# Kernel tuning notes

Measured on AMD Instinct MI355X. Metric: run time of the kernel, lower is better.

Reference implementation:

```python
import jax, jax.numpy as jnp
import numpy as np

T = 2048          # tokens (single-sequence prefill)
HID = 4096        # hidden_size
NH = 32           # num attention heads
NKV = 8           # num kv heads (GQA)
HD = 128          # head_dim
QKV_OUT = (NH + 2 * NKV) * HD  # 6144
THETA = 10000.0
SCALING = HD ** -0.5


def setup_inputs() -> dict:
    key = jax.random.key(0)
    ks = jax.random.split(key, 8)
    positions = jnp.arange(T, dtype=jnp.int32)
    # per-token int8 quantized hidden states (symmetric, [-127,127])
    q_act = jax.random.randint(ks[0], (T, HID), -127, 128, dtype=jnp.int32)
    # per-token dynamic activation scale
    act_scale = jax.random.uniform(ks[1], (T,), jnp.float32) * 0.01 + 0.001
    # int4 weights stored unsigned [0,15] with per-output-channel scale & zero point
    w_qkv_q = jax.random.randint(ks[2], (QKV_OUT, HID), 0, 16, dtype=jnp.int32)
    w_qkv_scale = jax.random.uniform(ks[3], (QKV_OUT,), jnp.float32) * 0.01 + 0.001
    w_qkv_zero = jax.random.uniform(ks[4], (QKV_OUT,), jnp.float32) * 2.0 + 7.0
    w_o_q = jax.random.randint(ks[5], (HID, HID), 0, 16, dtype=jnp.int32)
    w_o_scale = jax.random.uniform(ks[6], (HID,), jnp.float32) * 0.01 + 0.001
    w_o_zero = jax.random.uniform(ks[7], (HID,), jnp.float32) * 2.0 + 7.0
    return dict(positions=positions, q_act=q_act, act_scale=act_scale,
                w_qkv_q=w_qkv_q, w_qkv_scale=w_qkv_scale, w_qkv_zero=w_qkv_zero,
                w_o_q=w_o_q, w_o_scale=w_o_scale, w_o_zero=w_o_zero)


def w4a8_linear(qa_f, s_a, a_sum, qw, s_w, z_w):
    # y[t,o] = s_a[t]*s_w[o] * ( (qa @ qw^T)[t,o] - z_w[o]*sum_j qa[t,j] )
    acc = jnp.matmul(qa_f, qw.astype(jnp.float32).T)  # [T, O]
    return (s_a[:, None] * s_w[None, :]) * (acc - z_w[None, :] * a_sum[:, None])


def apply_rope(x, positions):
    # neox-style RoPE over full head_dim
    half = HD // 2
    inv_freq = THETA ** (-jnp.arange(0, half, dtype=jnp.float32) / half * 1.0)
    inv_freq = 1.0 / (THETA ** (jnp.arange(0, HD, 2, dtype=jnp.float32) / HD))
    freqs = positions.astype(jnp.float32)[:, None] * inv_freq[None, :]  # [T, HD/2]
    cos = jnp.cos(freqs)[:, None, :]
    sin = jnp.sin(freqs)[:, None, :]
    x1, x2 = x[..., :half], x[..., half:]
    return jnp.concatenate([x1 * cos - x2 * sin, x2 * cos + x1 * sin], axis=-1)


def dynamic_quant_with_sum(x):
    # per-token symmetric int8 dynamic quantization + fused sum
    s = jnp.maximum(jnp.max(jnp.abs(x), axis=-1), 1e-8) / 127.0  # [T]
    q = jnp.clip(jnp.round(x / s[:, None]), -127, 127)
    return q, s, jnp.sum(q, axis=-1)


def reference(positions, q_act, act_scale, w_qkv_q, w_qkv_scale, w_qkv_zero,
              w_o_q, w_o_scale, w_o_zero):
    qa_f = q_act.astype(jnp.float32)
    a_sum = jnp.sum(qa_f, axis=-1)  # fused activation sum
    qkv = w4a8_linear(qa_f, act_scale, a_sum, w_qkv_q, w_qkv_scale, w_qkv_zero)
    q, k, v = jnp.split(qkv, [NH * HD, NH * HD + NKV * HD], axis=-1)
    q = q.reshape(T, NH, HD)
    k = k.reshape(T, NKV, HD)
    v = v.reshape(T, NKV, HD)
    q = apply_rope(q, positions)
    k = apply_rope(k, positions)
    # GQA: repeat kv heads
    rep = NH // NKV
    k = jnp.repeat(k, rep, axis=1)  # [T, NH, HD]
    v = jnp.repeat(v, rep, axis=1)
    scores = jnp.einsum('qhd,khd->hqk', q, k) * SCALING  # [NH, T, T]
    causal = jnp.tril(jnp.ones((T, T), dtype=bool))
    scores = jnp.where(causal[None], scores, -jnp.inf)
    probs = jax.nn.softmax(scores, axis=-1)
    attn = jnp.einsum('hqk,khd->qhd', probs, v).reshape(T, NH * HD)
    # invoke_quant_fuse_sum: dynamic per-token quantization of attn output
    q2, s2, sum2 = dynamic_quant_with_sum(attn)
    out = w4a8_linear(q2, s2, sum2, w_o_q, w_o_scale, w_o_zero)
    return out
```

## Files before the change

kernel.cpp:

```cpp
#include <hip/hip_runtime.h>

#define T 2048
#define HID 4096
#define NH 32
#define NKV 8
#define HD 128
#define QKV_OUT ((NH + 2*NKV) * HD)
#define SCALING 0.08838834764831843f
#define QS2 0.12751744954f
#define DEFER_THR 10.0f
#define ROPE_C 0.20762050593046014f

typedef __attribute__((ext_vector_type(8))) short bfrag;
typedef __attribute__((ext_vector_type(4))) float ffrag;
typedef __attribute__((ext_vector_type(4))) int  ifrag;
typedef __attribute__((ext_vector_type(16))) char c16;

__device__ __forceinline__ short f2bf(float f) {
  unsigned u = __builtin_bit_cast(unsigned, f);
  u += 0x7fffu + ((u >> 16) & 1u);
  return (short)(u >> 16);
}

__device__ __forceinline__ void split2(float x, short& hi, short& lo) {
  unsigned u = __builtin_bit_cast(unsigned, x);
  unsigned uh = u + (0x7fffu + ((u >> 16) & 1u));
  hi = (short)(uh >> 16);
  float fh = __builtin_bit_cast(float, uh & 0xffff0000u);
  float r = x - fh;
  unsigned ur = __builtin_bit_cast(unsigned, r);
  ur += 0x7fffu + ((ur >> 16) & 1u);
  lo = (short)(ur >> 16);
}

__device__ __forceinline__ void gload_lds16(const void* g, void* l) {
  __builtin_amdgcn_global_load_lds(
      (const __attribute__((address_space(1))) unsigned int*)g,
      (__attribute__((address_space(3))) unsigned int*)l, 16, 0, 0);
}

__global__ __launch_bounds__(256)
void asum_conv(const int* __restrict__ qact, float* __restrict__ a_sum,
               char* __restrict__ a_i8) {
  __shared__ int red[256];
  const int t = blockIdx.x, tid = threadIdx.x;
  const int* row = qact + (size_t)t * HID + tid * 16;
  int s = 0;
  c16 o;
#pragma unroll
  for (int i = 0; i < 4; i++) {
    int4 v = *(const int4*)(row + i * 4);
    s += v.x + v.y + v.z + v.w;
    o[i*4+0] = (char)v.x; o[i*4+1] = (char)v.y;
    o[i*4+2] = (char)v.z; o[i*4+3] = (char)v.w;
  }
  *(c16*)(a_i8 + (size_t)t * HID + tid * 16) = o;
  red[tid] = s; __syncthreads();
  for (int off = 128; off > 0; off >>= 1) {
    if (tid < off) red[tid] += red[tid + off];
    __syncthreads();
  }
  if (tid == 0) a_sum[t] = (float)red[0];
}

__global__ __launch_bounds__(256)
void conv_i2c(const int* __restrict__ src, char* __restrict__ dst, int n16) {
  int idx = blockIdx.x * 256 + threadIdx.x;
  if (idx >= n16) return;
  const int4* s4 = (const int4*)src + (size_t)idx * 4;
  c16 o;
#pragma unroll
  for (int j = 0; j < 4; j++) {
    int4 v = s4[j];
    o[j*4+0] = (char)v.x; o[j*4+1] = (char)v.y;
    o[j*4+2] = (char)v.z; o[j*4+3] = (char)v.w;
  }
  *(c16*)(dst + (size_t)idx * 16) = o;
}

__global__ __launch_bounds__(256)
void gemm_i8(const char* __restrict__ A, const char* __restrict__ W,
             const float* __restrict__ s_a, const float* __restrict__ asum,
             const float* __restrict__ s_w, const float* __restrict__ z_w,
             float* __restrict__ C, int M, int N, int K) {
  __shared__ __align__(16) char As[128 * 64];
  __shared__ __align__(16) char Bs[128 * 64];
  const int tid = threadIdx.x;
  const int lane = tid & 63;
  const int quad = lane >> 4, l15 = lane & 15;
  const int wave = tid >> 6;
  const int wm = (wave >> 1) * 64, wn = (wave & 1) * 64;
  const int bm = blockIdx.y * 128, bn = blockIdx.x * 128;
  const int sr = tid >> 2, sc = (tid & 3) * 16;

  ifrag acc[4][4];
#pragma unroll
  for (int mi = 0; mi < 4; mi++)
#pragma unroll
    for (int ni = 0; ni < 4; ni++)
      acc[mi][ni] = (ifrag){0, 0, 0, 0};

  for (int k0 = 0; k0 < K; k0 += 64) {
#pragma unroll
    for (int it = 0; it < 2; it++) {
      gload_lds16(A + (size_t)(bm + it * 64 + sr) * K + k0 + sc,
                  &As[it * 4096 + wave * 1024]);
      gload_lds16(W + (size_t)(bn + it * 64 + sr) * K + k0 + sc,
                  &Bs[it * 4096 + wave * 1024]);
    }
    __syncthreads();

    ifrag af[4], bfv[4];
#pragma unroll
    for (int mi = 0; mi < 4; mi++)
      af[mi] = *(const ifrag*)&As[(wm + mi * 16 + l15) * 64 + quad * 16];
#pragma unroll
    for (int ni = 0; ni < 4; ni++)
      bfv[ni] = *(const ifrag*)&Bs[(wn + ni * 16 + l15) * 64 + quad * 16];
#pragma unroll
    for (int mi = 0; mi < 4; mi++)
#pragma unroll
      for (int ni = 0; ni < 4; ni++)
        acc[mi][ni] = __builtin_amdgcn_mfma_i32_16x16x64_i8(
            af[mi], bfv[ni], acc[mi][ni], 0, 0, 0);
    __syncthreads();
  }

#pragma unroll
  for (int mi = 0; mi < 4; mi++) {
    int row0 = bm + wm + mi * 16 + quad * 4;
#pragma unroll
    for (int r = 0; r < 4; r++) {
      int row = row0 + r;
      float sa = s_a[row], av = asum[row];
#pragma unroll
      for (int ni = 0; ni < 4; ni++) {
        int col = bn + wn + ni * 16 + l15;
        C[(size_t)row * N + col] = (sa * s_w[col]) * ((float)acc[mi][ni][r] - z_w[col] * av);
      }
    }
  }
}

__global__ __launch_bounds__(256)
void split_kv(float* __restrict__ qkv, const int* __restrict__ positions,
              short* __restrict__ Kh, short* __restrict__ Kl,
              short* __restrict__ Vth) {
  __shared__ __align__(16) short Vh_lds[128 * 72];
  const int y = blockIdx.y;
  const int t0 = blockIdx.x * 64;
  const int tid = threadIdx.x;

  if (y >= NKV) {
    const int h = y - NKV;
#pragma unroll
    for (int it = 0; it < 4; it++) {
      int c = tid + 256 * it;
      int key = c >> 4, dc = c & 15;
      float* qr = qkv + (size_t)(t0 + key) * QKV_OUT + (size_t)h * HD;
      float4 a = *(const float4*)(qr + dc * 4);
      float4 b = *(const float4*)(qr + dc * 4 + 64);
      float av[4] = {a.x, a.y, a.z, a.w};
      float bv[4] = {b.x, b.y, b.z, b.w};
      float pos = (float)positions[t0 + key];
#pragma unroll
      for (int jj = 0; jj < 4; jj++) {
        float fr = pos * exp2f(-ROPE_C * (float)(dc * 4 + jj));
        float sn, cs; sincosf(fr, &sn, &cs);
        float x1 = av[jj], x2 = bv[jj];
        av[jj] = x1 * cs - x2 * sn;
        bv[jj] = x2 * cs + x1 * sn;
      }
      *(float4*)(qr + dc * 4)      = make_float4(av[0], av[1], av[2], av[3]);
      *(float4*)(qr + dc * 4 + 64) = make_float4(bv[0], bv[1], bv[2], bv[3]);
    }
    return;
  }

  const int kvh = y;
#pragma unroll
  for (int it = 0; it < 4; it++) {
    int c = tid + 256 * it;
    int key = c >> 4, dc = c & 15;
    const int t = t0 + key;
    const float* kr = qkv + (size_t)t * QKV_OUT
                      + (size_t)NH * HD + (size_t)kvh * HD;
    float4 a = *(const float4*)(kr + dc * 4);
    float4 b = *(const float4*)(kr + dc * 4 + 64);
    float av[4] = {a.x, a.y, a.z, a.w};
    float bv[4] = {b.x, b.y, b.z, b.w};
    float pos = (float)positions[t];
    short4 ha, la, hb, lb;
    short hh, ll;
#pragma unroll
    for (int jj = 0; jj < 4; jj++) {
      float fr = pos * exp2f(-ROPE_C * (float)(dc * 4 + jj));
      float sn, cs; sincosf(fr, &sn, &cs);
      float x1 = av[jj], x2 = bv[jj];
      float r1 = x1 * cs - x2 * sn;
      float r2 = x2 * cs + x1 * sn;
      split2(r1, hh, ll); ((short*)&ha)[jj] = hh; ((short*)&la)[jj] = ll;
      split2(r2, hh, ll); ((short*)&hb)[jj] = hh; ((short*)&lb)[jj] = ll;
    }
    const int uu = ((dc >> 1) ^ t) & 7;
    const int h4 = (dc & 1) * 4;
    size_t base = (size_t)kvh * T * HD + (size_t)t * HD;
    *(short4*)(Kh + base + uu * 8 + h4) = ha;
    *(short4*)(Kl + base + uu * 8 + h4) = la;
    *(short4*)(Kh + base + (8 + uu) * 8 + h4) = hb;
    *(short4*)(Kl + base + (8 + uu) * 8 + h4) = lb;
  }
#pragma unroll
  for (int i = 0; i < 8; i++) {
    int c = tid + 256 * i;
    int key = c >> 5, dc = c & 31;
    float4 f = *(const float4*)(qkv + (size_t)(t0 + key) * QKV_OUT
                                + (size_t)(NH + NKV) * HD + (size_t)kvh * HD + dc * 4);
    Vh_lds[(dc*4+0)*72 + key] = f2bf(f.x);
    Vh_lds[(dc*4+1)*72 + key] = f2bf(f.y);
    Vh_lds[(dc*4+2)*72 + key] = f2bf(f.z);
    Vh_lds[(dc*4+3)*72 + key] = f2bf(f.w);
  }
  __syncthreads();
#pragma unroll
  for (int i = 0; i < 2; i++) {
    int c = tid + 256 * i;
    int row = c >> 2, cc = c & 3;
    int sd = (row >> 1) & 3;
    size_t o = (size_t)kvh * HD * T + (size_t)row * T + t0 + ((cc ^ sd)) * 8;
    *(bfrag*)(Vth + o) = *(const bfrag*)&Vh_lds[row * 72 + cc * 8];
  }
#pragma unroll
  for (int i = 0; i < 2; i++) {
    int c = tid + 256 * i;
    int row = c >> 2, cc = c & 3;
    int sd = (row >> 1) & 3;
    size_t o = (size_t)kvh * HD * T + (size_t)row * T + t0 + 32 + ((cc ^ sd)) * 8;
    *(bfrag*)(Vth + o) = *(const bfrag*)&Vh_lds[row * 72 + 32 + cc * 8];
  }
}

__global__ __launch_bounds__(256)
void attn_kernel(const float* __restrict__ qkv,
                 const short* __restrict__ Kh, const short* __restrict__ Kl,
                 const short* __restrict__ Vth,
                 float* __restrict__ attn) {
  __shared__ __align__(16) short Ksh[2][32 * 128];
  __shared__ __align__(16) short Ksl[2][32 * 128];
  __shared__ __align__(16) short Vsh[2][128 * 32];
  __shared__ __align__(16) short Psh[4 * 16 * 40];

  const int kvh = blockIdx.x & 7;
  const int pair = blockIdx.x >> 3;
  const int tid = threadIdx.x;
  const int lane = tid & 63;
  const int wv = tid >> 6;
  const int l15 = lane & 15, quad = lane >> 4;
  const int h = kvh * 4 + wv;
  short* Pw = Psh + wv * 16 * 40;

  const short* KhB = Kh + (size_t)kvh * T * HD;
  const short* KlB = Kl + (size_t)kvh * T * HD;
  const short* VhB = Vth + (size_t)kvh * HD * T;

  const int offK0 = (tid >> 4) * 128 + (tid & 15) * 8;
  const int offK1 = offK0 + 16 * 128;
  const int offV0 = (tid >> 2) * T + (tid & 3) * 8;
  const int offV1 = offV0 + 64 * T;
  const int wv1k = wv * 1024;

  auto stage = [&](int k0, int b) {
    const short* khs = KhB + (size_t)k0 * HD;
    const short* kls = KlB + (size_t)k0 * HD;
    const short* vs  = VhB + k0;
    gload_lds16(khs + offK0, (char*)&Ksh[b][0] + wv1k);
    gload_lds16(khs + offK1, (char*)&Ksh[b][0] + 4096 + wv1k);
    gload_lds16(kls + offK0, (char*)&Ksl[b][0] + wv1k);
    gload_lds16(kls + offK1, (char*)&Ksl[b][0] + 4096 + wv1k);
    gload_lds16(vs + offV0, (char*)&Vsh[b][0] + wv1k);
    gload_lds16(vs + offV1, (char*)&Vsh[b][0] + 4096 + wv1k);
  };

  const int sdv = (l15 >> 1) & 3;
  const int vq8 = (quad ^ sdv) * 8;
  int uuk[4];
#pragma unroll
  for (int kc = 0; kc < 4; kc++) {
    int s = 4 * kc + quad;
    uuk[kc] = ((s & 8) | ((s ^ l15) & 7)) * 8;
  }

  bfrag ones;
#pragma unroll
  for (int j = 0; j < 8; j++) ones[j] = (short)0x3f80;

  for (int pass = 0; pass < 2; pass++) {
    const int qt = pass ? pair : 127 - pair;
    const int q0 = qt * 16;
    const int nk = (q0 >> 5) + 1;

    bfrag qh[4], ql[4];
    const float* qrow = qkv + (size_t)(q0 + l15) * QKV_OUT + (size_t)h * HD;
#pragma unroll
    for (int kc = 0; kc < 4; kc++) {
      float4 f0 = *(const float4*)(qrow + kc * 32 + quad * 8);
      float4 f1 = *(const float4*)(qrow + kc * 32 + quad * 8 + 4);
      float fv[8] = {f0.x, f0.y, f0.z, f0.w, f1.x, f1.y, f1.z, f1.w};
#pragma unroll
      for (int j = 0; j < 8; j++) {
        short hi, lo; split2(fv[j] * QS2, hi, lo);
        qh[kc][j] = hi; ql[kc][j] = lo;
      }
    }

    ffrag o[8], ol;
    ol = (ffrag){0.f, 0.f, 0.f, 0.f};
#pragma unroll
    for (int n = 0; n < 8; n++) o[n] = (ffrag){0.f, 0.f, 0.f, 0.f};
    float m_i[4] = {-1e30f, -1e30f, -1e30f, -1e30f};

    stage(0, 0);
    asm volatile("s_waitcnt vmcnt(0)" ::: "memory");
    __builtin_amdgcn_s_barrier();

    int cur = 0;
    for (int kt = 0; kt < nk; kt++) {
      const int k0 = kt << 5;
      if (kt + 1 < nk) stage(k0 + 32, cur ^ 1);

      const short* ksh = &Ksh[cur][0];
      const short* ksl = &Ksl[cur][0];
      const short* vsh = &Vsh[cur][0];

      ffrag s[2];
      s[0] = (ffrag){0.f,0.f,0.f,0.f}; s[1] = (ffrag){0.f,0.f,0.f,0.f};
#pragma unroll
      for (int kc = 0; kc < 4; kc++) {
#pragma unroll
        for (int n = 0; n < 2; n++) {
          const int rb = (n * 16 + l15) * 128 + uuk[kc];
          bfrag bh = *(const bfrag*)&ksh[rb];
          bfrag bl = *(const bfrag*)&ksl[rb];
          s[n] = __builtin_amdgcn_mfma_f32_16x16x32_bf16(qh[kc], bh, s[n], 0,0,0);
          s[n] = __builtin_amdgcn_mfma_f32_16x16x32_bf16(qh[kc], bl, s[n], 0,0,0);
          s[n] = __builtin_amdgcn_mfma_f32_16x16x32_bf16(ql[kc], bh, s[n], 0,0,0);
        }
      }
      const bool lastkt = (kt == nk - 1);
      float sv[2][4];
#pragma unroll
      for (int n = 0; n < 2; n++)
#pragma unroll
        for (int r = 0; r < 4; r++) {
          float v = s[n][r];
          if (lastkt) {
            int key = k0 + n * 16 + l15;
            int row = q0 + quad * 4 + r;
            if (key > row) v = -1e30f;
          }
          sv[n][r] = v;
        }
      float lm[4];
      bool trig = false;
#pragma unroll
      for (int r = 0; r < 4; r++) {
        lm[r] = fmaxf(sv[0][r], sv[1][r]);
        trig = trig || (lm[r] > m_i[r] + DEFER_THR);
      }
      if (__any(trig)) {
#pragma unroll
        for (int r = 0; r < 4; r++) {
          float m2 = lm[r];
          m2 = fmaxf(m2, __shfl_xor(m2, 1));
          m2 = fmaxf(m2, __shfl_xor(m2, 2));
          m2 = fmaxf(m2, __shfl_xor(m2, 4));
          m2 = fmaxf(m2, __shfl_xor(m2, 8));
          float mn = fmaxf(m_i[r], m2);
          float a = exp2f(m_i[r] - mn);
          m_i[r] = mn;
          ol[r] *= a;
#pragma unroll
          for (int n = 0; n < 8; n++) o[n][r] *= a;
        }
      }
#pragma unroll
      for (int n = 0; n < 2; n++)
#pragma unroll
        for (int r = 0; r < 4; r++) {
          float p = exp2f(sv[n][r] - m_i[r]);
          Pw[(quad*4 + r) * 40 + n*16 + l15] = f2bf(p);
        }
      bfrag ph = *(const bfrag*)&Pw[l15 * 40 + quad * 8];
      ol = __builtin_amdgcn_mfma_f32_16x16x32_bf16(ph, ones, ol, 0,0,0);
#pragma unroll
      for (int n = 0; n < 8; n++) {
        bfrag vh = *(const bfrag*)&vsh[(n * 16 + l15) * 32 + vq8];
        o[n] = __builtin_amdgcn_mfma_f32_16x16x32_bf16(ph, vh, o[n], 0,0,0);
      }

      asm volatile("s_waitcnt vmcnt(0)" ::: "memory");
      __builtin_amdgcn_s_barrier();
      cur ^= 1;
    }

    float inv[4];
#pragma unroll
    for (int r = 0; r < 4; r++) inv[r] = 1.f / ol[r];
#pragma unroll
    for (int n = 0; n < 8; n++)
#pragma unroll
      for (int r = 0; r < 4; r++) {
        int row = q0 + quad * 4 + r;
        attn[(size_t)row * HID + (size_t)h * HD + n * 16 + l15] = o[n][r] * inv[r];
      }
  }
}

__global__ __launch_bounds__(256)
void quant_kernel(const float* __restrict__ x, char* __restrict__ q2,
                  float* __restrict__ s2, float* __restrict__ sum2) {
  __shared__ float red[256];
  const int t = blockIdx.x, tid = threadIdx.x;
  const float* row = x + (size_t)t * HID;
  float4 v[4];
  float m = 0.f;
#pragma unroll
  for (int i = 0; i < 4; i++) {
    v[i] = *(const float4*)(row + tid * 16 + i * 4);
    m = fmaxf(m, fmaxf(fmaxf(fabsf(v[i].x), fabsf(v[i].y)),
                       fmaxf(fabsf(v[i].z), fabsf(v[i].w))));
  }
  red[tid] = m; __syncthreads();
  for (int off = 128; off > 0; off >>= 1) {
    if (tid < off) red[tid] = fmaxf(red[tid], red[tid + off]);
    __syncthreads();
  }
  float s = fmaxf(red[0], 1e-8f) / 127.f;
  __syncthreads();
  float ssum = 0.f;
  c16 o;
#pragma unroll
  for (int i = 0; i < 4; i++) {
    float q;
    q = fminf(127.f, fmaxf(-127.f, rintf(v[i].x / s))); ssum += q; o[i*4+0] = (char)(int)q;
    q = fminf(127.f, fmaxf(-127.f, rintf(v[i].y / s))); ssum += q; o[i*4+1] = (char)(int)q;
    q = fminf(127.f, fmaxf(-127.f, rintf(v[i].z / s))); ssum += q; o[i*4+2] = (char)(int)q;
    q = fminf(127.f, fmaxf(-127.f, rintf(v[i].w / s))); ssum += q; o[i*4+3] = (char)(int)q;
  }
  *(c16*)(q2 + (size_t)t * HID + tid * 16) = o;
  red[tid] = ssum; __syncthreads();
  for (int off = 128; off > 0; off >>= 1) {
    if (tid < off) red[tid] += red[tid + off];
    __syncthreads();
  }
  if (tid == 0) { s2[t] = s; sum2[t] = red[0]; }
}

extern "C" void kernel_launch(void* const* d_in, const int* in_sizes, int n_in,
                              void* d_out, int out_size, void* d_ws, size_t ws_size,
                              hipStream_t stream) {
  const int*   positions   = (const int*)d_in[0];
  const int*   q_act       = (const int*)d_in[1];
  const float* act_scale   = (const float*)d_in[2];
  const int*   w_qkv_q     = (const int*)d_in[3];
  const float* w_qkv_scale = (const float*)d_in[4];
  const float* w_qkv_zero  = (const float*)d_in[5];
  const int*   w_o_q       = (const int*)d_in[6];
  const float* w_o_scale   = (const float*)d_in[7];
  const float* w_o_zero    = (const float*)d_in[8];
  float* out = (float*)d_out;

  size_t off = 0;
  auto alloc = [&](size_t bytes) -> void* {
    void* p = (char*)d_ws + off;
    off += (bytes + 255) & ~(size_t)255;
    return p;
  };
  float* qkv   = (float*)alloc((size_t)T * QKV_OUT * 4);
  char*  act8  = (char*)alloc((size_t)T * HID);
  char*  w8    = (char*)alloc((size_t)QKV_OUT * HID);
  short* Kh    = (short*)alloc((size_t)NKV * T * HD * 2);
  short* Kl    = (short*)alloc((size_t)NKV * T * HD * 2);
  short* Vth   = (short*)alloc((size_t)NKV * T * HD * 2);
  float* a_sum = (float*)alloc(T * 4);
  float* s2    = (float*)alloc(T * 4);
  float* sum2  = (float*)alloc(T * 4);
  (void)ws_size;

  asum_conv<<<T, 256, 0, stream>>>(q_act, a_sum, act8);
  conv_i2c<<<(QKV_OUT * HID / 16 + 255) / 256, 256, 0, stream>>>(
      w_qkv_q, w8, QKV_OUT * HID / 16);
  gemm_i8<<<dim3(QKV_OUT / 128, T / 128), 256, 0, stream>>>(
      act8, w8, act_scale, a_sum, w_qkv_scale, w_qkv_zero, qkv, T, QKV_OUT, HID);
  split_kv<<<dim3(T / 64, NKV + NH), 256, 0, stream>>>(qkv, positions, Kh, Kl, Vth);
  attn_kernel<<<dim3(512), 256, 0, stream>>>(qkv, Kh, Kl, Vth, out);
  conv_i2c<<<(HID * HID / 16 + 255) / 256, 256, 0, stream>>>(
      w_o_q, w8, HID * HID / 16);
  quant_kernel<<<T, 256, 0, stream>>>(out, act8, s2, sum2);
  gemm_i8<<<dim3(HID / 128, T / 128), 256, 0, stream>>>(
      act8, w8, s2, sum2, w_o_scale, w_o_zero, out, T, HID, HID);
}
```

Baseline: 522.3 us.

## Double GEMM K-tile to 128 with XOR-swizzled int8 layout; precompute RoPE table

```diff
diff --git a/kernel.cpp b/kernel.cpp
--- a/kernel.cpp
+++ b/kernel.cpp
@@ -40,6 +40,16 @@
 }
 
 __global__ __launch_bounds__(256)
+void rope_table(float2* __restrict__ tab) {
+  int idx = blockIdx.x * 256 + threadIdx.x;
+  int p = idx >> 6, j = idx & 63;
+  float fr = (float)p * exp2f(-ROPE_C * (float)j);
+  float sn, cs; sincosf(fr, &sn, &cs);
+  tab[idx] = make_float2(cs, sn);
+}
+
+
+__global__ __launch_bounds__(256)
 void asum_conv(const int* __restrict__ qact, float* __restrict__ a_sum,
                char* __restrict__ a_i8) {
   __shared__ int red[256];
@@ -54,7 +64,8 @@
     o[i*4+0] = (char)v.x; o[i*4+1] = (char)v.y;
     o[i*4+2] = (char)v.z; o[i*4+3] = (char)v.w;
   }
-  *(c16*)(a_i8 + (size_t)t * HID + tid * 16) = o;
+  const int chunk = (tid & ~7) | ((tid & 7) ^ (t & 7));
+  *(c16*)(a_i8 + (size_t)t * HID + chunk * 16) = o;
   red[tid] = s; __syncthreads();
   for (int off = 128; off > 0; off >>= 1) {
     if (tid < off) red[tid] += red[tid + off];
@@ -75,7 +86,8 @@
     o[j*4+0] = (char)v.x; o[j*4+1] = (char)v.y;
     o[j*4+2] = (char)v.z; o[j*4+3] = (char)v.w;
   }
-  *(c16*)(dst + (size_t)idx * 16) = o;
+  const int idxp = (idx & ~7) | ((idx & 7) ^ ((idx >> 8) & 7));
+  *(c16*)(dst + (size_t)idxp * 16) = o;
 }
 
 __global__ __launch_bounds__(256)
@@ -83,15 +95,15 @@
              const float* __restrict__ s_a, const float* __restrict__ asum,
              const float* __restrict__ s_w, const float* __restrict__ z_w,
              float* __restrict__ C, int M, int N, int K) {
-  __shared__ __align__(16) char As[128 * 64];
-  __shared__ __align__(16) char Bs[128 * 64];
+  __shared__ __align__(16) char As[128 * 128];
+  __shared__ __align__(16) char Bs[128 * 128];
   const int tid = threadIdx.x;
   const int lane = tid & 63;
   const int quad = lane >> 4, l15 = lane & 15;
   const int wave = tid >> 6;
   const int wm = (wave >> 1) * 64, wn = (wave & 1) * 64;
   const int bm = blockIdx.y * 128, bn = blockIdx.x * 128;
-  const int sr = tid >> 2, sc = (tid & 3) * 16;
+  const int sr = tid >> 3, sc = (tid & 7) * 16;
 
   ifrag acc[4][4];
 #pragma unroll
@@ -100,29 +112,36 @@
     for (int ni = 0; ni < 4; ni++)
       acc[mi][ni] = (ifrag){0, 0, 0, 0};
 
-  for (int k0 = 0; k0 < K; k0 += 64) {
-#pragma unroll
-    for (int it = 0; it < 2; it++) {
-      gload_lds16(A + (size_t)(bm + it * 64 + sr) * K + k0 + sc,
-                  &As[it * 4096 + wave * 1024]);
-      gload_lds16(W + (size_t)(bn + it * 64 + sr) * K + k0 + sc,
-                  &Bs[it * 4096 + wave * 1024]);
+  const int scol0 = ((quad)     ^ (l15 & 7)) * 16;
+  const int scol1 = ((4 + quad) ^ (l15 & 7)) * 16;
+
+  for (int k0 = 0; k0 < K; k0 += 128) {
+#pragma unroll
+    for (int j = 0; j < 4; j++) {
+      gload_lds16(A + (size_t)(bm + j * 32 + sr) * K + k0 + sc,
+                  &As[j * 4096 + tid * 16]);
+      gload_lds16(W + (size_t)(bn + j * 32 + sr) * K + k0 + sc,
+                  &Bs[j * 4096 + tid * 16]);
     }
     __syncthreads();
 
-    ifrag af[4], bfv[4];
-#pragma unroll
-    for (int mi = 0; mi < 4; mi++)
-      af[mi] = *(const ifrag*)&As[(wm + mi * 16 + l15) * 64 + quad * 16];
-#pragma unroll
-    for (int ni = 0; ni < 4; ni++)
-      bfv[ni] = *(const ifrag*)&Bs[(wn + ni * 16 + l15) * 64 + quad * 16];
-#pragma unroll
-    for (int mi = 0; mi < 4; mi++)
+#pragma unroll
+    for (int ks = 0; ks < 2; ks++) {
+      const int scol = ks ? scol1 : scol0;
+      ifrag af[4], bfv[4];
+#pragma unroll
+      for (int mi = 0; mi < 4; mi++)
+        af[mi] = *(const ifrag*)&As[(wm + mi * 16 + l15) * 128 + scol];
 #pragma unroll
       for (int ni = 0; ni < 4; ni++)
-        acc[mi][ni] = __builtin_amdgcn_mfma_i32_16x16x64_i8(
-            af[mi], bfv[ni], acc[mi][ni], 0, 0, 0);
+        bfv[ni] = *(const ifrag*)&Bs[(wn + ni * 16 + l15) * 128 + scol];
+#pragma unroll
+      for (int mi = 0; mi < 4; mi++)
+#pragma unroll
+        for (int ni = 0; ni < 4; ni++)
+          acc[mi][ni] = __builtin_amdgcn_mfma_i32_16x16x64_i8(
+              af[mi], bfv[ni], acc[mi][ni], 0, 0, 0);
+    }
     __syncthreads();
   }
 
@@ -144,6 +163,7 @@
 
 __global__ __launch_bounds__(256)
 void split_kv(float* __restrict__ qkv, const int* __restrict__ positions,
+              const float2* __restrict__ tab,
               short* __restrict__ Kh, short* __restrict__ Kl,
               short* __restrict__ Vth) {
   __shared__ __align__(16) short Vh_lds[128 * 72];
@@ -162,11 +182,10 @@
       float4 b = *(const float4*)(qr + dc * 4 + 64);
       float av[4] = {a.x, a.y, a.z, a.w};
       float bv[4] = {b.x, b.y, b.z, b.w};
-      float pos = (float)positions[t0 + key];
+      const float2* tr = tab + (size_t)positions[t0 + key] * 64 + dc * 4;
 #pragma unroll
       for (int jj = 0; jj < 4; jj++) {
-        float fr = pos * exp2f(-ROPE_C * (float)(dc * 4 + jj));
-        float sn, cs; sincosf(fr, &sn, &cs);
+        float cs = tr[jj].x, sn = tr[jj].y;
         float x1 = av[jj], x2 = bv[jj];
         av[jj] = x1 * cs - x2 * sn;
         bv[jj] = x2 * cs + x1 * sn;
@@ -189,13 +208,12 @@
     float4 b = *(const float4*)(kr + dc * 4 + 64);
     float av[4] = {a.x, a.y, a.z, a.w};
     float bv[4] = {b.x, b.y, b.z, b.w};
-    float pos = (float)positions[t];
+    const float2* tr = tab + (size_t)positions[t] * 64 + dc * 4;
     short4 ha, la, hb, lb;
     short hh, ll;
 #pragma unroll
     for (int jj = 0; jj < 4; jj++) {
-      float fr = pos * exp2f(-ROPE_C * (float)(dc * 4 + jj));
-      float sn, cs; sincosf(fr, &sn, &cs);
+      float cs = tr[jj].x, sn = tr[jj].y;
       float x1 = av[jj], x2 = bv[jj];
       float r1 = x1 * cs - x2 * sn;
       float r2 = x2 * cs + x1 * sn;
@@ -447,7 +465,8 @@
     q = fminf(127.f, fmaxf(-127.f, rintf(v[i].z / s))); ssum += q; o[i*4+2] = (char)(int)q;
     q = fminf(127.f, fmaxf(-127.f, rintf(v[i].w / s))); ssum += q; o[i*4+3] = (char)(int)q;
   }
-  *(c16*)(q2 + (size_t)t * HID + tid * 16) = o;
+  const int chunk = (tid & ~7) | ((tid & 7) ^ (t & 7));
+  *(c16*)(q2 + (size_t)t * HID + chunk * 16) = o;
   red[tid] = ssum; __syncthreads();
   for (int off = 128; off > 0; off >>= 1) {
     if (tid < off) red[tid] += red[tid + off];
@@ -485,14 +504,17 @@
   float* a_sum = (float*)alloc(T * 4);
   float* s2    = (float*)alloc(T * 4);
   float* sum2  = (float*)alloc(T * 4);
+  float2* tab  = (float2*)alloc((size_t)T * 64 * 8);
   (void)ws_size;
 
+  rope_table<<<T * 64 / 256, 256, 0, stream>>>(tab);
   asum_conv<<<T, 256, 0, stream>>>(q_act, a_sum, act8);
   conv_i2c<<<(QKV_OUT * HID / 16 + 255) / 256, 256, 0, stream>>>(
       w_qkv_q, w8, QKV_OUT * HID / 16);
   gemm_i8<<<dim3(QKV_OUT / 128, T / 128), 256, 0, stream>>>(
       act8, w8, act_scale, a_sum, w_qkv_scale, w_qkv_zero, qkv, T, QKV_OUT, HID);
-  split_kv<<<dim3(T / 64, NKV + NH), 256, 0, stream>>>(qkv, positions, Kh, Kl, Vth);
+  split_kv<<<dim3(T / 64, NKV + NH), 256, 0, stream>>>(
+      qkv, positions, tab, Kh, Kl, Vth);
   attn_kernel<<<dim3(512), 256, 0, stream>>>(qkv, Kh, Kl, Vth, out);
   conv_i2c<<<(HID * HID / 16 + 255) / 256, 256, 0, stream>>>(
       w_o_q, w8, HID * HID / 16);
```

After: 489.4 us. 1.07x faster.
